# Kernel tuning notes

Hardware: AMD Instinct MI355X
Metric: run time of the kernel (lower is better)

Reference implementation:

```python
import jax, jax.numpy as jnp
import numpy as np
from jax import lax

B, T, D = 4, 4096, 1024
H, d = 4, 64
EPS = 1e-6

def pos_unit(x):
    # positive feature map (elu+1) normalized to unit L2 norm along feature dim
    p = jax.nn.elu(x) + 1.0
    return p / (jnp.linalg.norm(p, axis=-1, keepdims=True) + EPS)

def setup_inputs() -> dict:
    key = jax.random.key(0)
    ks = jax.random.split(key, 5)
    s_in = 1.0 / np.sqrt(D)
    s_hd = 1.0 / np.sqrt(H * d)
    return {
        "x": jax.random.normal(ks[0], (B, T, D), dtype=jnp.float32),
        "Wq": jax.random.normal(ks[1], (H * d, D), dtype=jnp.float32) * s_in,
        "Wk": jax.random.normal(ks[2], (H * d, D), dtype=jnp.float32) * s_in,
        "Wv": jax.random.normal(ks[3], (H * d, D), dtype=jnp.float32) * s_in,
        "Wo": jax.random.normal(ks[4], (D, H * d), dtype=jnp.float32) * s_hd,
    }

def reference(x, Wq, Wk, Wv, Wo):
    Bx, Tx, Dx = x.shape
    q = (x @ Wq.T).reshape(Bx, Tx, H, d)
    k = (x @ Wk.T).reshape(Bx, Tx, H, d)
    v = (x @ Wv.T).reshape(Bx, Tx, H, d)
    q = pos_unit(q)
    k = pos_unit(k)
    # time-major for scan: [T, B, H, d]
    qT = jnp.transpose(q, (1, 0, 2, 3))
    kT = jnp.transpose(k, (1, 0, 2, 3))
    vT = jnp.transpose(v, (1, 0, 2, 3))
    kv0 = jnp.zeros((Bx, H, d, d), dtype=x.dtype)  # [B,H,j,d]
    kc0 = jnp.zeros((Bx, H, d), dtype=x.dtype)

    def step(carry, inp):
        kv_cum, k_cum = carry
        qt, kt, vt = inp  # each [B,H,d]
        kv_cum = kv_cum + jnp.einsum('bhd,bhj->bhjd', kt, vt)
        k_cum = k_cum + kt
        num = jnp.einsum('bhd,bhjd->bhj', qt, kv_cum)
        den = jnp.einsum('bhd,bhd->bh', qt, k_cum)[..., None] + EPS
        return (kv_cum, k_cum), num / den

    (kv_f, kc_f), yT = lax.scan(step, (kv0, kc0), (qT, kT, vT))
    y = jnp.transpose(yT, (1, 0, 2, 3)).reshape(Bx, Tx, H * d)
    y = y @ Wo.T
    return y, kv_f, kc_f
```

## Files before the change

kernel.cpp:

```cpp
#include <hip/hip_runtime.h>
#include <hip/hip_bf16.h>
#include <math.h>

#define T_SEQ   4096
#define NB      4
#define NH      4
#define DH      64
#define DM      1024
#define MR      16384
#define NQKV    768
#define CH      64
#define NCH     64
#define SST     4160
#define BHN     16

typedef __attribute__((ext_vector_type(4))) float          f32x4;
typedef __attribute__((ext_vector_type(8))) short          s16x8;
typedef __attribute__((ext_vector_type(4))) unsigned short u16x4;

__device__ __forceinline__ float bf2f(unsigned short u) {
  union { unsigned int i; float f; } c; c.i = ((unsigned int)u) << 16; return c.f;
}
__device__ __forceinline__ unsigned short f2bf(float f) {
  union { float f; unsigned int i; } c; c.f = f;
  unsigned int i = c.i;
  return (unsigned short)((i + 0x7fffu + ((i >> 16) & 1u)) >> 16);
}
__device__ __forceinline__ s16x8 pack8(f32x4 lo, f32x4 hi) {
  s16x8 r;
  r[0] = (short)f2bf(lo.x); r[1] = (short)f2bf(lo.y);
  r[2] = (short)f2bf(lo.z); r[3] = (short)f2bf(lo.w);
  r[4] = (short)f2bf(hi.x); r[5] = (short)f2bf(hi.y);
  r[6] = (short)f2bf(hi.z); r[7] = (short)f2bf(hi.w);
  return r;
}
__device__ __forceinline__ void gl_lds16(const unsigned short* g, unsigned short* l) {
  __builtin_amdgcn_global_load_lds(
      (const __attribute__((address_space(1))) unsigned int*)g,
      (__attribute__((address_space(3))) unsigned int*)l, 16, 0, 0);
}

__global__ __launch_bounds__(256) void convert_kernel(
    const float* __restrict__ X,
    const float* __restrict__ Wq, const float* __restrict__ Wk,
    const float* __restrict__ Wv,
    unsigned short* __restrict__ Xb, unsigned short* __restrict__ Wb)
{
  const long long NX = 16777216LL;
  const long long NW = 786432LL;
  const long long total = NX + NW;
  const long long stride = (long long)gridDim.x * 256 * 8;
  for (long long i = ((long long)blockIdx.x * 256 + threadIdx.x) * 8;
       i < total; i += stride) {
    const float* src;
    unsigned short* dst;
    if (i < NX) { src = X + i; dst = Xb + i; }
    else {
      const long long e = i - NX;
      const int w = (int)(e >> 18);
      const long long rr = e & 262143LL;
      src = (w == 0 ? Wq : w == 1 ? Wk : Wv) + rr;
      dst = Wb + e;
    }
    const f32x4 lo = *(const f32x4*)src;
    const f32x4 hi = *(const f32x4*)(src + 4);
    *(s16x8*)dst = pack8(lo, hi);
  }
}

__global__ __launch_bounds__(256, 2) void gemm_qkv_kernel(
    const unsigned short* __restrict__ Xb,
    const unsigned short* __restrict__ Wb,
    unsigned short* __restrict__ C)
{
  constexpr int K = DM;
  constexpr int N = NQKV;
  __shared__ __align__(16) unsigned short sA[128 * 32];
  __shared__ __align__(16) unsigned short sB[128 * 32];

  const int tid  = threadIdx.x;
  const int wave = tid >> 6;
  const int lane = tid & 63;
  const int quad = lane >> 4;
  const int l16  = lane & 15;
  const int wm = (wave >> 1) * 64;
  const int wn = (wave & 1) * 64;

  const int row0 = blockIdx.x * 128;
  const int bn   = blockIdx.y;
  const int srow = tid >> 2;
  const int scol = ((tid & 3) ^ (srow & 3)) * 8;
  const unsigned short* Ag = Xb + (size_t)(row0     + srow) * K + scol;
  const unsigned short* Bg = Wb + (size_t)(bn * 128 + srow) * K + scol;
  unsigned short* sAp = sA + tid * 8;
  unsigned short* sBp = sB + tid * 8;

  const int ra = (quad ^ (l16 & 3)) * 8;

  f32x4 acc[4][4];
  #pragma unroll
  for (int i = 0; i < 4; i++)
    #pragma unroll
    for (int j = 0; j < 4; j++) acc[i][j] = (f32x4){0.f, 0.f, 0.f, 0.f};

  for (int kt = 0; kt < K; kt += 32) {
    __syncthreads();
    gl_lds16(Ag + kt,                  sAp);
    gl_lds16(Ag + kt + (size_t)64 * K, sAp + 2048);
    gl_lds16(Bg + kt,                  sBp);
    gl_lds16(Bg + kt + (size_t)64 * K, sBp + 2048);
    __syncthreads();
    s16x8 af[4], bw[4];
    #pragma unroll
    for (int i = 0; i < 4; i++)
      af[i] = *(const s16x8*)(sA + (wm + i * 16 + l16) * 32 + ra);
    #pragma unroll
    for (int j = 0; j < 4; j++)
      bw[j] = *(const s16x8*)(sB + (wn + j * 16 + l16) * 32 + ra);
    #pragma unroll
    for (int i = 0; i < 4; i++)
      #pragma unroll
      for (int j = 0; j < 4; j++)
        acc[i][j] = __builtin_amdgcn_mfma_f32_16x16x32_bf16(af[i], bw[j], acc[i][j], 0, 0, 0);
  }

  const int colb = bn * 128 + wn;
  if (bn < 4) {
    #pragma unroll
    for (int i = 0; i < 4; i++) {
      const int r = row0 + wm + i * 16 + quad * 4;
      #pragma unroll
      for (int g = 0; g < 4; g++) {
        float p[4];
        float ss = 0.f;
        #pragma unroll
        for (int j = 0; j < 4; j++) {
          const float a = acc[i][j][g];
          p[j] = a > 0.f ? a + 1.f : __expf(a);
          ss += p[j] * p[j];
        }
        ss += __shfl_xor(ss, 1, 64);
        ss += __shfl_xor(ss, 2, 64);
        ss += __shfl_xor(ss, 4, 64);
        ss += __shfl_xor(ss, 8, 64);
        const float inv = 1.f / (sqrtf(ss) + 1e-6f);
        #pragma unroll
        for (int j = 0; j < 4; j++)
          C[(size_t)(r + g) * N + colb + j * 16 + l16] = f2bf(p[j] * inv);
      }
    }
  } else {
    #pragma unroll
    for (int i = 0; i < 4; i++) {
      const int r = row0 + wm + i * 16 + quad * 4;
      #pragma unroll
      for (int j = 0; j < 4; j++) {
        const int cc = colb + j * 16 + l16;
        #pragma unroll
        for (int g = 0; g < 4; g++)
          C[(size_t)(r + g) * N + cc] = f2bf(acc[i][j][g]);
      }
    }
  }
}

__global__ __launch_bounds__(256, 2) void gemm_out_kernel(
    const unsigned short* __restrict__ Y,
    const float* __restrict__ Wo,
    float* __restrict__ Out)
{
  constexpr int K = 256;
  constexpr int N = DM;
  __shared__ __align__(16) unsigned short sA[128 * 32];
  __shared__ __align__(16) unsigned short sB[128 * 32];

  const int tid  = threadIdx.x;
  const int wave = tid >> 6;
  const int lane = tid & 63;
  const int quad = lane >> 4;
  const int l16  = lane & 15;
  const int wm = (wave >> 1) * 64;
  const int wn = (wave & 1) * 64;

  const int row0  = blockIdx.x * 128;
  const int bcol0 = blockIdx.y * 128;

  const int srow = tid >> 2;
  const int scol = ((tid & 3) ^ (srow & 3)) * 8;
  const unsigned short* Ag = Y  + (size_t)(row0  + srow) * K + scol;
  const float*          Bg = Wo + (size_t)(bcol0 + srow) * K + scol;
  unsigned short* sAp = sA + tid * 8;
  unsigned short* sBp = sB + tid * 8;

  const int ra = (quad ^ (l16 & 3)) * 8;

  f32x4 acc[4][4];
  #pragma unroll
  for (int i = 0; i < 4; i++)
    #pragma unroll
    for (int j = 0; j < 4; j++) acc[i][j] = (f32x4){0.f, 0.f, 0.f, 0.f};

  for (int kt = 0; kt < K; kt += 32) {
    const f32x4 b0l = *(const f32x4*)(Bg + kt);
    const f32x4 b0h = *(const f32x4*)(Bg + kt + 4);
    const f32x4 b1l = *(const f32x4*)(Bg + kt + (size_t)64 * K);
    const f32x4 b1h = *(const f32x4*)(Bg + kt + (size_t)64 * K + 4);
    __syncthreads();
    gl_lds16(Ag + kt,                  sAp);
    gl_lds16(Ag + kt + (size_t)64 * K, sAp + 2048);
    *(s16x8*)sBp          = pack8(b0l, b0h);
    *(s16x8*)(sBp + 2048) = pack8(b1l, b1h);
    __syncthreads();
    s16x8 af[4], bw[4];
    #pragma unroll
    for (int i = 0; i < 4; i++)
      af[i] = *(const s16x8*)(sA + (wm + i * 16 + l16) * 32 + ra);
    #pragma unroll
    for (int j = 0; j < 4; j++)
      bw[j] = *(const s16x8*)(sB + (wn + j * 16 + l16) * 32 + ra);
    #pragma unroll
    for (int i = 0; i < 4; i++)
      #pragma unroll
      for (int j = 0; j < 4; j++)
        acc[i][j] = __builtin_amdgcn_mfma_f32_16x16x32_bf16(af[i], bw[j], acc[i][j], 0, 0, 0);
  }

  #pragma unroll
  for (int i = 0; i < 4; i++) {
    const int r = row0 + wm + i * 16 + quad * 4;
    #pragma unroll
    for (int j = 0; j < 4; j++) {
      const int cc = bcol0 + wn + j * 16 + l16;
      #pragma unroll
      for (int g = 0; g < 4; g++)
        Out[(size_t)(r + g) * N + cc] = acc[i][j][g];
    }
  }
}

__global__ __launch_bounds__(256) void chunk_sums_kernel(
    const unsigned short* __restrict__ qkv,
    float* __restrict__ cs)
{
  const int blk = blockIdx.x;
  const int bh = blk >> 6, c = blk & 63;
  const int b = bh >> 2, h = bh & 3;
  __shared__ __align__(16) unsigned short sKt[64 * 64];
  __shared__ __align__(16) unsigned short sVt[64 * 64];
  __shared__ float sPart[4 * 64];
  const int wave = threadIdx.x >> 6, lane = threadIdx.x & 63;
  const int quad = lane >> 4, l16 = lane & 15;
  const size_t rowbase = ((size_t)b * T_SEQ + (size_t)c * CH) * NQKV + h * DH;

  float kacc = 0.f;
  #pragma unroll 4
  for (int tt = 0; tt < 16; tt++) {
    const int t = tt * 4 + wave;
    const unsigned short* r = qkv + rowbase + (size_t)t * NQKV;
    const unsigned short ku = r[256 + lane];
    const unsigned short vu = r[512 + lane];
    kacc += bf2f(ku);
    const int sw = (lane & 7) << 3;
    sKt[lane * 64 + (t ^ sw)] = ku;
    sVt[lane * 64 + (t ^ sw)] = vu;
  }
  sPart[wave * 64 + lane] = kacc;
  __syncthreads();

  const int wr = (wave >> 1) * 32;
  const int wc = (wave & 1) * 32;
  f32x4 acc[2][2];
  #pragma unroll
  for (int i = 0; i < 2; i++)
    #pragma unroll
    for (int j = 0; j < 2; j++) acc[i][j] = (f32x4){0.f, 0.f, 0.f, 0.f};

  #pragma unroll
  for (int ks = 0; ks < 2; ks++) {
    const int grp = ks * 4 + quad;
    s16x8 ak[2], bv[2];
    #pragma unroll
    for (int i = 0; i < 2; i++) {
      const int rk = wr + i * 16 + l16;
      ak[i] = *(const s16x8*)(sKt + rk * 64 + ((grp ^ (rk & 7)) << 3));
    }
    #pragma unroll
    for (int j = 0; j < 2; j++) {
      const int rj = wc + j * 16 + l16;
      bv[j] = *(const s16x8*)(sVt + rj * 64 + ((grp ^ (rj & 7)) << 3));
    }
    #pragma unroll
    for (int i = 0; i < 2; i++)
      #pragma unroll
      for (int j = 0; j < 2; j++)
        acc[i][j] = __builtin_amdgcn_mfma_f32_16x16x32_bf16(ak[i], bv[j], acc[i][j], 0, 0, 0);
  }

  float* o = cs + (size_t)blk * SST;
  #pragma unroll
  for (int i = 0; i < 2; i++)
    #pragma unroll
    for (int j = 0; j < 2; j++)
      #pragma unroll
      for (int g = 0; g < 4; g++) {
        const int dd = wr + i * 16 + quad * 4 + g;
        const int jj = wc + j * 16 + l16;
        o[dd * 64 + jj] = acc[i][j][g];
      }
  if (threadIdx.x < 64)
    o[4096 + threadIdx.x] = sPart[threadIdx.x] + sPart[64 + threadIdx.x]
                          + sPart[128 + threadIdx.x] + sPart[192 + threadIdx.x];
}

__global__ __launch_bounds__(256) void scan_kernel(
    float* __restrict__ cs, float* __restrict__ outTail)
{
  const int gid = blockIdx.x * 256 + threadIdx.x;
  const int bh = gid / SST;
  const int e  = gid - bh * SST;
  float run = 0.f;
  size_t idx = (size_t)bh * NCH * SST + e;
  for (int c = 0; c < NCH; c++, idx += SST) {
    const float v = cs[idx];
    cs[idx] = run;
    run += v;
  }
  if (e < 4096) {
    const int dd = e >> 6, j = e & 63;
    outTail[(size_t)bh * 4096 + j * 64 + dd] = run;
  } else {
    const int dd = e - 4096;
    outTail[BHN * 4096 + (size_t)bh * 64 + dd] = run;
  }
}

__global__ __launch_bounds__(256, 4) void chunk_out_kernel(
    const unsigned short* __restrict__ qkv,
    const float* __restrict__ st,
    unsigned short* __restrict__ yatt)
{
  const int blk = blockIdx.x;
  const int bh = blk >> 6;
  const int c  = blk & 63;
  const int b = bh >> 2, h = bh & 3;

  __shared__ __align__(16) unsigned short sQ [64 * 64];
  __shared__ __align__(16) unsigned short sKA[64 * 64];
  __shared__ __align__(16) unsigned short sVt[64 * 64];
  __shared__ __align__(16) unsigned short sSt[64 * 64];
  __shared__ float sKc[64];
  __shared__ float sDen[64];

  const int tid  = threadIdx.x;
  const int wave = tid >> 6, lane = tid & 63;
  const int quad = lane >> 4, l16 = lane & 15;
  const size_t rowbase = ((size_t)b * T_SEQ + (size_t)c * CH) * NQKV + h * DH;

  #pragma unroll
  for (int p = 0; p < 2; p++) {
    const int e  = p * 2048 + tid * 8;
    const int t  = e >> 6;
    const int c0 = e & 56;
    const int sc = c0 ^ ((t & 7) << 3);
    const unsigned short* src = qkv + rowbase + (size_t)t * NQKV + sc;
    gl_lds16(src,       sQ  + e);
    gl_lds16(src + 256, sKA + e);
  }
  #pragma unroll 4
  for (int tt = 0; tt < 16; tt++) {
    const int t = tt * 4 + wave;
    sVt[lane * 64 + (t ^ ((lane & 7) << 3))] =
        qkv[rowbase + (size_t)t * NQKV + 512 + lane];
  }
  const float* stp = st + (size_t)blk * SST;
  for (int i = tid; i < 1024; i += 256) {
    const f32x4 s4 = ((const f32x4*)stp)[i];
    const int d = i >> 4, j0 = (i & 15) << 2;
    #pragma unroll
    for (int g = 0; g < 4; g++) {
      const int j = j0 + g;
      sSt[j * 64 + (d ^ ((j & 7) << 3))] = f2bf(s4[g]);
    }
  }
  if (tid < 64) sKc[tid] = stp[4096 + tid];
  __syncthreads();

  const int wr = (wave >> 1) * 32;
  const int wc = (wave & 1) * 32;

  f32x4 accA[2][2];
  #pragma unroll
  for (int i = 0; i < 2; i++)
    #pragma unroll
    for (int j = 0; j < 2; j++) accA[i][j] = (f32x4){0.f, 0.f, 0.f, 0.f};

  #pragma unroll
  for (int ks = 0; ks < 2; ks++) {
    const int grp = ks * 4 + quad;
    s16x8 aq[2], bk[2];
    #pragma unroll
    for (int i = 0; i < 2; i++) {
      const int rq = wr + i * 16 + l16;
      aq[i] = *(const s16x8*)(sQ + rq * 64 + ((grp ^ (rq & 7)) << 3));
    }
    #pragma unroll
    for (int j = 0; j < 2; j++) {
      const int rk = wc + j * 16 + l16;
      bk[j] = *(const s16x8*)(sKA + rk * 64 + ((grp ^ (rk & 7)) << 3));
    }
    #pragma unroll
    for (int i = 0; i < 2; i++)
      #pragma unroll
      for (int j = 0; j < 2; j++)
        accA[i][j] = __builtin_amdgcn_mfma_f32_16x16x32_bf16(aq[i], bk[j], accA[i][j], 0, 0, 0);
  }
  __syncthreads();

  #pragma unroll
  for (int i = 0; i < 2; i++)
    #pragma unroll
    for (int j = 0; j < 2; j++)
      #pragma unroll
      for (int g = 0; g < 4; g++) {
        const int t = wr + i * 16 + quad * 4 + g;
        const int s = wc + j * 16 + l16;
        const float av = (s <= t) ? accA[i][j][g] : 0.f;
        sKA[t * 64 + (s ^ ((t & 7) << 3))] = f2bf(av);
      }
  __syncthreads();

  {
    const int t = tid >> 2, p = tid & 3;
    const int sw = (t & 7) << 3;
    float s = 0.f;
    #pragma unroll
    for (int e = 0; e < 16; e++) {
      const int d = p * 16 + e;
      s += bf2f(sKA[t * 64 + d]);
      s += bf2f(sQ[t * 64 + (d ^ sw)]) * sKc[d];
    }
    s += __shfl_xor(s, 1, 64);
    s += __shfl_xor(s, 2, 64);
    if (p == 0) sDen[t] = s + 1e-6f;
  }
  __syncthreads();

  f32x4 acc[2][2];
  #pragma unroll
  for (int i = 0; i < 2; i++)
    #pragma unroll
    for (int j = 0; j < 2; j++) acc[i][j] = (f32x4){0.f, 0.f, 0.f, 0.f};

  #pragma unroll
  for (int ks = 0; ks < 2; ks++) {
    const int grp = ks * 4 + quad;
    s16x8 aq[2], bs[2];
    #pragma unroll
    for (int i = 0; i < 2; i++) {
      const int rq = wr + i * 16 + l16;
      aq[i] = *(const s16x8*)(sQ + rq * 64 + ((grp ^ (rq & 7)) << 3));
    }
    #pragma unroll
    for (int j = 0; j < 2; j++) {
      const int rj = wc + j * 16 + l16;
      bs[j] = *(const s16x8*)(sSt + rj * 64 + ((grp ^ (rj & 7)) << 3));
    }
    #pragma unroll
    for (int i = 0; i < 2; i++)
      #pragma unroll
      for (int j = 0; j < 2; j++)
        acc[i][j] = __builtin_amdgcn_mfma_f32_16x16x32_bf16(aq[i], bs[j], acc[i][j], 0, 0, 0);
  }
  #pragma unroll
  for (int ks = 0; ks < 2; ks++) {
    const int grp = ks * 4 + quad;
    s16x8 aa[2], bv[2];
    #pragma unroll
    for (int i = 0; i < 2; i++) {
      const int rt = wr + i * 16 + l16;
      aa[i] = *(const s16x8*)(sKA + rt * 64 + ((grp ^ (rt & 7)) << 3));
    }
    #pragma unroll
    for (int j = 0; j < 2; j++) {
      const int rj = wc + j * 16 + l16;
      bv[j] = *(const s16x8*)(sVt + rj * 64 + ((grp ^ (rj & 7)) << 3));
    }
    #pragma unroll
    for (int i = 0; i < 2; i++)
      #pragma unroll
      for (int j = 0; j < 2; j++)
        acc[i][j] = __builtin_amdgcn_mfma_f32_16x16x32_bf16(aa[i], bv[j], acc[i][j], 0, 0, 0);
  }

  #pragma unroll
  for (int i = 0; i < 2; i++)
    #pragma unroll
    for (int g = 0; g < 4; g++) {
      const int t = wr + i * 16 + quad * 4 + g;
      const float inv = 1.f / sDen[t];
      #pragma unroll
      for (int j = 0; j < 2; j++) {
        const int jj = wc + j * 16 + l16;
        const size_t o = ((size_t)b * T_SEQ + (size_t)c * CH + t) * 256 + h * 64 + jj;
        yatt[o] = f2bf(acc[i][j][g] * inv);
      }
    }
}

extern "C" void kernel_launch(void* const* d_in, const int* in_sizes, int n_in,
                              void* d_out, int out_size, void* d_ws, size_t ws_size,
                              hipStream_t stream) {
  const float* X  = (const float*)d_in[0];
  const float* Wq = (const float*)d_in[1];
  const float* Wk = (const float*)d_in[2];
  const float* Wv = (const float*)d_in[3];
  const float* Wo = (const float*)d_in[4];
  float* out = (float*)d_out;

  unsigned short* qkvb = (unsigned short*)d_out;
  unsigned short* Xb   = (unsigned short*)((char*)d_out + 25165824ull);
  unsigned short* Wb   = Xb + 16777216;
  float* outTail = out + 16777216;
  float*          cs   = (float*)d_ws;
  unsigned short* yatt = (unsigned short*)((char*)d_ws + 17039360ull);

  convert_kernel   <<<4096,         256, 0, stream>>>(X, Wq, Wk, Wv, Xb, Wb);
  gemm_qkv_kernel  <<<dim3(128, 6), 256, 0, stream>>>(Xb, Wb, qkvb);
  chunk_sums_kernel<<<BHN * NCH,    256, 0, stream>>>(qkvb, cs);
  scan_kernel      <<<(BHN * SST) / 256, 256, 0, stream>>>(cs, outTail);
  chunk_out_kernel <<<BHN * NCH,    256, 0, stream>>>(qkvb, cs, yatt);
  gemm_out_kernel  <<<dim3(128, 8), 256, 0, stream>>>(yatt, Wo, out);
}
```

Measured before the change: 199.3 us.

## Double-buffer LDS tiles in QKV and output GEMMs, preload Wo slab

Both GEMM kernels now double-buffer the activation tiles in shared memory. Each iteration issues the next k-slice's global-to-LDS loads before running the MFMAs on the current slice, which removes one barrier per iteration and overlaps loads with compute. The output GEMM also loads its whole 128x256 Wo slab once, converted to bf16 with an XOR swizzle, instead of re-reading and converting fp32 weights every k-step. The cost is more LDS per block (the out kernel reaches about 80KB), which may reduce occupancy.

```diff
diff --git a/kernel.cpp b/kernel.cpp
--- a/kernel.cpp
+++ b/kernel.cpp
@@ -75,8 +75,8 @@
 {
   constexpr int K = DM;
   constexpr int N = NQKV;
-  __shared__ __align__(16) unsigned short sA[128 * 32];
-  __shared__ __align__(16) unsigned short sB[128 * 32];
+  __shared__ __align__(16) unsigned short sA[2][128 * 32];
+  __shared__ __align__(16) unsigned short sB[2][128 * 32];
 
   const int tid  = threadIdx.x;
   const int wave = tid >> 6;
@@ -92,8 +92,6 @@
   const int scol = ((tid & 3) ^ (srow & 3)) * 8;
   const unsigned short* Ag = Xb + (size_t)(row0     + srow) * K + scol;
   const unsigned short* Bg = Wb + (size_t)(bn * 128 + srow) * K + scol;
-  unsigned short* sAp = sA + tid * 8;
-  unsigned short* sBp = sB + tid * 8;
 
   const int ra = (quad ^ (l16 & 3)) * 8;
 
@@ -103,25 +101,34 @@
     #pragma unroll
     for (int j = 0; j < 4; j++) acc[i][j] = (f32x4){0.f, 0.f, 0.f, 0.f};
 
+  gl_lds16(Ag,                  &sA[0][tid * 8]);
+  gl_lds16(Ag + (size_t)64 * K, &sA[0][tid * 8 + 2048]);
+  gl_lds16(Bg,                  &sB[0][tid * 8]);
+  gl_lds16(Bg + (size_t)64 * K, &sB[0][tid * 8 + 2048]);
+  __syncthreads();
+
+  int cur = 0;
   for (int kt = 0; kt < K; kt += 32) {
-    __syncthreads();
-    gl_lds16(Ag + kt,                  sAp);
-    gl_lds16(Ag + kt + (size_t)64 * K, sAp + 2048);
-    gl_lds16(Bg + kt,                  sBp);
-    gl_lds16(Bg + kt + (size_t)64 * K, sBp + 2048);
-    __syncthreads();
+    if (kt + 32 < K) {
+      gl_lds16(Ag + kt + 32,                  &sA[cur ^ 1][tid * 8]);
+      gl_lds16(Ag + kt + 32 + (size_t)64 * K, &sA[cur ^ 1][tid * 8 + 2048]);
+      gl_lds16(Bg + kt + 32,                  &sB[cur ^ 1][tid * 8]);
+      gl_lds16(Bg + kt + 32 + (size_t)64 * K, &sB[cur ^ 1][tid * 8 + 2048]);
+    }
     s16x8 af[4], bw[4];
     #pragma unroll
     for (int i = 0; i < 4; i++)
-      af[i] = *(const s16x8*)(sA + (wm + i * 16 + l16) * 32 + ra);
+      af[i] = *(const s16x8*)(&sA[cur][(wm + i * 16 + l16) * 32 + ra]);
     #pragma unroll
     for (int j = 0; j < 4; j++)
-      bw[j] = *(const s16x8*)(sB + (wn + j * 16 + l16) * 32 + ra);
+      bw[j] = *(const s16x8*)(&sB[cur][(wn + j * 16 + l16) * 32 + ra]);
     #pragma unroll
     for (int i = 0; i < 4; i++)
       #pragma unroll
       for (int j = 0; j < 4; j++)
         acc[i][j] = __builtin_amdgcn_mfma_f32_16x16x32_bf16(af[i], bw[j], acc[i][j], 0, 0, 0);
+    __syncthreads();
+    cur ^= 1;
   }
 
   const int colb = bn * 128 + wn;
@@ -171,8 +178,8 @@
 {
   constexpr int K = 256;
   constexpr int N = DM;
-  __shared__ __align__(16) unsigned short sA[128 * 32];
-  __shared__ __align__(16) unsigned short sB[128 * 32];
+  __shared__ __align__(16) unsigned short sB[128 * 256];
+  __shared__ __align__(16) unsigned short sA[2][128 * 32];
 
   const int tid  = threadIdx.x;
   const int wave = tid >> 6;
@@ -187,10 +194,21 @@
 
   const int srow = tid >> 2;
   const int scol = ((tid & 3) ^ (srow & 3)) * 8;
-  const unsigned short* Ag = Y  + (size_t)(row0  + srow) * K + scol;
-  const float*          Bg = Wo + (size_t)(bcol0 + srow) * K + scol;
-  unsigned short* sAp = sA + tid * 8;
-  unsigned short* sBp = sB + tid * 8;
+  const unsigned short* Ag = Y + (size_t)(row0 + srow) * K + scol;
+
+  gl_lds16(Ag,                  &sA[0][tid * 8]);
+  gl_lds16(Ag + (size_t)64 * K, &sA[0][tid * 8 + 2048]);
+  #pragma unroll
+  for (int rr = 0; rr < 16; rr++) {
+    const int e   = rr * 2048 + tid * 8;
+    const int row = e >> 8;
+    const int g   = (e >> 3) & 31;
+    const float* src = Wo + (size_t)(bcol0 + row) * K + ((g ^ (row & 7)) << 3);
+    const f32x4 lo = *(const f32x4*)src;
+    const f32x4 hi = *(const f32x4*)(src + 4);
+    *(s16x8*)(sB + e) = pack8(lo, hi);
+  }
+  __syncthreads();
 
   const int ra = (quad ^ (l16 & 3)) * 8;
 
@@ -200,29 +218,30 @@
     #pragma unroll
     for (int j = 0; j < 4; j++) acc[i][j] = (f32x4){0.f, 0.f, 0.f, 0.f};
 
-  for (int kt = 0; kt < K; kt += 32) {
-    const f32x4 b0l = *(const f32x4*)(Bg + kt);
-    const f32x4 b0h = *(const f32x4*)(Bg + kt + 4);
-    const f32x4 b1l = *(const f32x4*)(Bg + kt + (size_t)64 * K);
-    const f32x4 b1h = *(const f32x4*)(Bg + kt + (size_t)64 * K + 4);
-    __syncthreads();
-    gl_lds16(Ag + kt,                  sAp);
-    gl_lds16(Ag + kt + (size_t)64 * K, sAp + 2048);
-    *(s16x8*)sBp          = pack8(b0l, b0h);
-    *(s16x8*)(sBp + 2048) = pack8(b1l, b1h);
-    __syncthreads();
+  int cur = 0;
+  for (int ks = 0; ks < 8; ks++) {
+    const int kt = ks * 32;
+    if (ks < 7) {
+      gl_lds16(Ag + kt + 32,                  &sA[cur ^ 1][tid * 8]);
+      gl_lds16(Ag + kt + 32 + (size_t)64 * K, &sA[cur ^ 1][tid * 8 + 2048]);
+    }
     s16x8 af[4], bw[4];
     #pragma unroll
     for (int i = 0; i < 4; i++)
-      af[i] = *(const s16x8*)(sA + (wm + i * 16 + l16) * 32 + ra);
-    #pragma unroll
-    for (int j = 0; j < 4; j++)
-      bw[j] = *(const s16x8*)(sB + (wn + j * 16 + l16) * 32 + ra);
+      af[i] = *(const s16x8*)(&sA[cur][(wm + i * 16 + l16) * 32 + ra]);
+    #pragma unroll
+    for (int j = 0; j < 4; j++) {
+      const int r = wn + j * 16 + l16;
+      const int g = (kt >> 3) + quad;
+      bw[j] = *(const s16x8*)(sB + r * 256 + ((g ^ (r & 7)) << 3));
+    }
     #pragma unroll
     for (int i = 0; i < 4; i++)
       #pragma unroll
       for (int j = 0; j < 4; j++)
         acc[i][j] = __builtin_amdgcn_mfma_f32_16x16x32_bf16(af[i], bw[j], acc[i][j], 0, 0, 0);
+    __syncthreads();
+    cur ^= 1;
   }
 
   #pragma unroll
```

Result: slower. 203.9 us (+2.3%).
